# Optimization experiments

Measured on AMD Instinct MI355X. Metric: run time of the kernel, lower is better.

## Reference

```python
import jax, jax.numpy as jnp
import numpy as np

NUM_CLUSTERS = 32


def setup_inputs() -> dict:
    key = jax.random.key(0)
    k1, k2 = jax.random.split(key)
    B, N, D = 16, 16384, 128
    x = jax.random.normal(k1, (B, N, D), dtype=jnp.float32)
    cluster_ids = jax.random.randint(k2, (B, N), 0, NUM_CLUSTERS, dtype=jnp.int32)
    return {"x": x, "cluster_ids": cluster_ids}


def reference(x, cluster_ids):
    # x: [B, N, D]; cluster_ids: [B, N] int labels in [0, C)
    C = NUM_CLUSTERS
    # One-hot cluster membership: [B, N, C]
    onehot = (cluster_ids[..., None] == jnp.arange(C, dtype=cluster_ids.dtype)).astype(x.dtype)
    counts = onehot.sum(axis=1)                       # [B, C]
    sums = jnp.einsum('bnc,bnd->bcd', onehot, x)      # segment sums [B, C, D]
    # Per-cluster mean; empty clusters -> zero rows (contribute 0 to off-diag Gram)
    means = sums / jnp.maximum(counts, 1.0)[..., None]
    # Pairwise |dot products| between cluster means: [B, C, C]
    gram = jnp.abs(jnp.einsum('bcd,bed->bce', means, means))
    # Strict upper-triangular sum (torch.triu(..., diagonal=1))
    triu_mask = jnp.triu(jnp.ones((C, C), dtype=x.dtype), k=1)
    triu_sum = jnp.sum(gram * triu_mask, axis=(1, 2))  # [B]
    # Number of valid (non-empty) clusters per batch
    valid = jnp.sum(counts > 0, axis=1).astype(x.dtype)
    denom = jnp.where(valid > 1, valid * (valid - 1.0) * 0.5, 1.0)
    return jnp.mean(triu_sum / denom)
```

## Files before the change

### kernel.cpp

```cpp
#include <hip/hip_runtime.h>
#include <hip/hip_bf16.h>

#define BB 16
#define NN 16384
#define DD 128
#define CC 32
#define CHUNKS 32
#define NBLK (BB * CHUNKS)
#define ROWS_PER_BLOCK (NN / CHUNKS)
#define ROWS_PER_WAVE  (ROWS_PER_BLOCK / 4)

#define P_SUMS 0
#define P_CNTS ((size_t)NBLK * CC * DD)
#define R_SUMS (P_CNTS + (size_t)NBLK * CC)
#define R_CNTS (R_SUMS + (size_t)BB * CC * DD)
#define LOSSP  (R_CNTS + (size_t)BB * CC)
#define WS_A_FLOATS (LOSSP + BB)

__global__ __launch_bounds__(256) void seg_sum_kernel(
    const float* __restrict__ x, const int* __restrict__ ids,
    float* __restrict__ outsums, float* __restrict__ outcnts, int mode) {
  __shared__ float lsum[4][CC * DD];
  __shared__ float lcnt[CC];
  __shared__ int   lcid[ROWS_PER_BLOCK];

  const int tid  = threadIdx.x;
  const int b    = blockIdx.y;
  const int row0 = blockIdx.x * ROWS_PER_BLOCK;
  const int lane = tid & 63;
  const int w    = tid >> 6;
  const int slot = b * CHUNKS + blockIdx.x;
  const int* __restrict__ idrow = ids + (size_t)b * NN;

  if (tid < CC) lcnt[tid] = 0.f;
  lcid[tid]       = idrow[row0 + tid];
  lcid[tid + 256] = idrow[row0 + tid + 256];
  {
    const float4 z4 = make_float4(0.f, 0.f, 0.f, 0.f);
#pragma unroll
    for (int i = 0; i < 16; ++i)
      *reinterpret_cast<float4*>(&lsum[w][(i * 64 + lane) * 4]) = z4;
  }
  __syncthreads();
  atomicAdd(&lcnt[lcid[tid]], 1.f);
  atomicAdd(&lcnt[lcid[tid + 256]], 1.f);

  const float2* __restrict__ x2 =
      reinterpret_cast<const float2*>(x + (size_t)b * NN * DD);
  const int wbase = w * ROWS_PER_WAVE;
  float* const slab = &lsum[w][0];

  float2 vA[16], vB[16];
  int cA[16], cB[16];

#define LOADG(V, C, g)                                                     \
  {                                                                        \
    _Pragma("unroll") for (int k = 0; k < 16; ++k) {                       \
      const int rl = wbase + (g) * 16 + k;                                 \
      V[k] = x2[(size_t)(row0 + rl) * 64 + lane];                          \
      C[k] = lcid[rl];                                                     \
    }                                                                      \
  }
#define RMWG(V, C)                                                         \
  {                                                                        \
    _Pragma("unroll") for (int k = 0; k < 16; ++k) {                       \
      float2* p = reinterpret_cast<float2*>(&slab[C[k] * DD + 2 * lane]);  \
      float2 old = *p;                                                     \
      *p = make_float2(old.x + V[k].x, old.y + V[k].y);                    \
    }                                                                      \
  }

  LOADG(vA, cA, 0)
#pragma unroll
  for (int i = 0; i < 3; ++i) {
    LOADG(vB, cB, 2 * i + 1)
    RMWG(vA, cA)
    LOADG(vA, cA, 2 * i + 2)
    RMWG(vB, cB)
  }
  LOADG(vB, cB, 7)
  RMWG(vA, cA)
  RMWG(vB, cB)
#undef LOADG
#undef RMWG
  __syncthreads();

  if (mode) {
    float* __restrict__ ps = outsums + (size_t)slot * CC * DD;
#pragma unroll
    for (int it = 0; it < 4; ++it) {
      const int i = (it * 256 + tid) * 4;
      float4 s0 = *reinterpret_cast<const float4*>(&lsum[0][i]);
      float4 s1 = *reinterpret_cast<const float4*>(&lsum[1][i]);
      float4 s2 = *reinterpret_cast<const float4*>(&lsum[2][i]);
      float4 s3 = *reinterpret_cast<const float4*>(&lsum[3][i]);
      float4 r = make_float4(s0.x + s1.x + s2.x + s3.x, s0.y + s1.y + s2.y + s3.y,
                             s0.z + s1.z + s2.z + s3.z, s0.w + s1.w + s2.w + s3.w);
      *reinterpret_cast<float4*>(&ps[i]) = r;
    }
    if (tid < CC) outcnts[slot * CC + tid] = lcnt[tid];
  } else {
    float* __restrict__ gs = outsums + (size_t)b * CC * DD;
    for (int i = tid; i < CC * DD; i += 256) {
      float s = lsum[0][i] + lsum[1][i] + lsum[2][i] + lsum[3][i];
      atomicAdd(&gs[i], s);
    }
    if (tid < CC) atomicAdd(&outcnts[b * CC + tid], lcnt[tid]);
  }
}

__global__ __launch_bounds__(256) void reduce_partials_kernel(
    const float* __restrict__ psums, const float* __restrict__ pcnts,
    float* __restrict__ rsums, float* __restrict__ rcnts) {
  const int j = blockIdx.x;
  const int b = j >> 4;
  const int e0 = (j & 15) * 256;
  const int tid = threadIdx.x;
  float s = 0.f;
#pragma unroll 8
  for (int c = 0; c < CHUNKS; ++c)
    s += psums[((size_t)(b * CHUNKS + c)) * CC * DD + e0 + tid];
  rsums[(size_t)b * CC * DD + e0 + tid] = s;
  if ((j & 15) == 0 && tid < CC) {
    float cs = 0.f;
#pragma unroll 8
    for (int c = 0; c < CHUNKS; ++c) cs += pcnts[(b * CHUNKS + c) * CC + tid];
    rcnts[b * CC + tid] = cs;
  }
}

#define MSTR 132
__global__ __launch_bounds__(512) void finish_kernel(
    const float* __restrict__ gsums, const float* __restrict__ gcounts,
    float* __restrict__ lossp, float* __restrict__ out, int mode) {
  __shared__ float mean[CC * MSTR];
  __shared__ float cnt[CC];
  __shared__ float red[512];

  const int b = blockIdx.x;
  const int tid = threadIdx.x;

  if (tid < CC) cnt[tid] = gcounts[b * CC + tid];
  __syncthreads();

  for (int i = tid; i < CC * DD; i += 512) {
    int c = i >> 7;
    int d = i & 127;
    mean[c * MSTR + d] = gsums[(size_t)b * CC * DD + i] / fmaxf(cnt[c], 1.f);
  }
  __syncthreads();

  float acc = 0.f;
  if (tid < (CC * (CC - 1)) / 2) {
    int c = 0, rem = tid;
    while (rem >= (CC - 1 - c)) { rem -= (CC - 1 - c); ++c; }
    int e = c + 1 + rem;
    const float4* mc = reinterpret_cast<const float4*>(&mean[c * MSTR]);
    const float4* me = reinterpret_cast<const float4*>(&mean[e * MSTR]);
    float dot = 0.f;
#pragma unroll 8
    for (int j = 0; j < DD / 4; ++j) {
      float4 a = mc[j], bb = me[j];
      dot += a.x * bb.x + a.y * bb.y + a.z * bb.z + a.w * bb.w;
    }
    acc = fabsf(dot);
  }

  red[tid] = acc;
  __syncthreads();
  for (int s = 256; s > 0; s >>= 1) {
    if (tid < s) red[tid] += red[tid + s];
    __syncthreads();
  }

  if (tid == 0) {
    float valid = 0.f;
    for (int c = 0; c < CC; ++c) valid += (cnt[c] > 0.f) ? 1.f : 0.f;
    float denom = (valid > 1.f) ? valid * (valid - 1.f) * 0.5f : 1.f;
    float v = red[0] / denom * (1.0f / BB);
    if (mode) lossp[b] = v;
    else atomicAdd(out, v);
  }
}

__global__ __launch_bounds__(64) void final_kernel(
    const float* __restrict__ lossp, float* __restrict__ out) {
  float v = (threadIdx.x < BB) ? lossp[threadIdx.x] : 0.f;
#pragma unroll
  for (int o = 8; o > 0; o >>= 1) v += __shfl_down(v, o, 16);
  if (threadIdx.x == 0) out[0] = v;
}

extern "C" void kernel_launch(void* const* d_in, const int* in_sizes, int n_in,
                              void* d_out, int out_size, void* d_ws, size_t ws_size,
                              hipStream_t stream) {
  const float* x   = (const float*)d_in[0];
  const int*   ids = (const int*)d_in[1];
  float* out = (float*)d_out;
  float* ws  = (float*)d_ws;

  dim3 grid1(CHUNKS, BB);
  if (ws_size >= WS_A_FLOATS * sizeof(float)) {
    float* psums = ws + P_SUMS;
    float* pcnts = ws + P_CNTS;
    float* rsums = ws + R_SUMS;
    float* rcnts = ws + R_CNTS;
    float* lossp = ws + LOSSP;
    seg_sum_kernel<<<grid1, 256, 0, stream>>>(x, ids, psums, pcnts, 1);
    reduce_partials_kernel<<<256, 256, 0, stream>>>(psums, pcnts, rsums, rcnts);
    finish_kernel<<<BB, 512, 0, stream>>>(rsums, rcnts, lossp, out, 1);
    final_kernel<<<1, 64, 0, stream>>>(lossp, out);
  } else {
    float* gsums   = ws;
    float* gcounts = gsums + (size_t)BB * CC * DD;
    const size_t wsb = ((size_t)BB * CC * DD + (size_t)BB * CC) * sizeof(float);
    hipMemsetAsync(d_ws, 0, wsb, stream);
    hipMemsetAsync(d_out, 0, sizeof(float), stream);
    seg_sum_kernel<<<grid1, 256, 0, stream>>>(x, ids, gsums, gcounts, 0);
    finish_kernel<<<BB, 512, 0, stream>>>(gsums, gcounts, nullptr, out, 0);
  }
}
```

Baseline: 40.90 us.

## Fuse partial reduction and final loss into one finish kernel with atomic counter

Removes the separate reduce_partials and final kernels. The finish kernel now sums the 32 chunk partials itself, with 16 blocks each reading 512 KB. The last block to finish, detected through an atomic counter that seg_sum resets, writes the output. This cuts two launches and an intermediate global round trip, but the partial reduction now runs on only 16 blocks instead of 256, so it has less memory parallelism.

```diff
diff --git a/kernel.cpp b/kernel.cpp
--- a/kernel.cpp
+++ b/kernel.cpp
@@ -12,14 +12,14 @@
 
 #define P_SUMS 0
 #define P_CNTS ((size_t)NBLK * CC * DD)
-#define R_SUMS (P_CNTS + (size_t)NBLK * CC)
-#define R_CNTS (R_SUMS + (size_t)BB * CC * DD)
-#define LOSSP  (R_CNTS + (size_t)BB * CC)
-#define WS_A_FLOATS (LOSSP + BB)
+#define LOSSP  (P_CNTS + (size_t)NBLK * CC)
+#define CTR    (LOSSP + BB)
+#define WS_A_FLOATS (CTR + 1)
 
 __global__ __launch_bounds__(256) void seg_sum_kernel(
     const float* __restrict__ x, const int* __restrict__ ids,
-    float* __restrict__ outsums, float* __restrict__ outcnts, int mode) {
+    float* __restrict__ outsums, float* __restrict__ outcnts,
+    int* __restrict__ counter, int mode) {
   __shared__ float lsum[4][CC * DD];
   __shared__ float lcnt[CC];
   __shared__ int   lcid[ROWS_PER_BLOCK];
@@ -99,6 +99,8 @@
       *reinterpret_cast<float4*>(&ps[i]) = r;
     }
     if (tid < CC) outcnts[slot * CC + tid] = lcnt[tid];
+    if (slot == 0 && tid == 0)
+      __hip_atomic_store(counter, 0, __ATOMIC_RELAXED, __HIP_MEMORY_SCOPE_AGENT);
   } else {
     float* __restrict__ gs = outsums + (size_t)b * CC * DD;
     for (int i = tid; i < CC * DD; i += 256) {
@@ -109,44 +111,43 @@
   }
 }
 
-__global__ __launch_bounds__(256) void reduce_partials_kernel(
+#define MSTR 132
+__global__ __launch_bounds__(512) void finish_fused_kernel(
     const float* __restrict__ psums, const float* __restrict__ pcnts,
-    float* __restrict__ rsums, float* __restrict__ rcnts) {
-  const int j = blockIdx.x;
-  const int b = j >> 4;
-  const int e0 = (j & 15) * 256;
+    float* __restrict__ lossp, int* __restrict__ counter,
+    float* __restrict__ out) {
+  __shared__ float mean[CC * MSTR];
+  __shared__ float cnt[CC];
+  __shared__ float red[512];
+
+  const int b = blockIdx.x;
   const int tid = threadIdx.x;
-  float s = 0.f;
-#pragma unroll 8
-  for (int c = 0; c < CHUNKS; ++c)
-    s += psums[((size_t)(b * CHUNKS + c)) * CC * DD + e0 + tid];
-  rsums[(size_t)b * CC * DD + e0 + tid] = s;
-  if ((j & 15) == 0 && tid < CC) {
+
+  if (tid < CC) {
     float cs = 0.f;
 #pragma unroll 8
     for (int c = 0; c < CHUNKS; ++c) cs += pcnts[(b * CHUNKS + c) * CC + tid];
-    rcnts[b * CC + tid] = cs;
-  }
-}
-
-#define MSTR 132
-__global__ __launch_bounds__(512) void finish_kernel(
-    const float* __restrict__ gsums, const float* __restrict__ gcounts,
-    float* __restrict__ lossp, float* __restrict__ out, int mode) {
-  __shared__ float mean[CC * MSTR];
-  __shared__ float cnt[CC];
-  __shared__ float red[512];
-
-  const int b = blockIdx.x;
-  const int tid = threadIdx.x;
-
-  if (tid < CC) cnt[tid] = gcounts[b * CC + tid];
-  __syncthreads();
-
-  for (int i = tid; i < CC * DD; i += 512) {
-    int c = i >> 7;
-    int d = i & 127;
-    mean[c * MSTR + d] = gsums[(size_t)b * CC * DD + i] / fmaxf(cnt[c], 1.f);
+    cnt[tid] = cs;
+  }
+
+  float4 a0 = make_float4(0.f, 0.f, 0.f, 0.f), a1 = a0;
+  const size_t base = (size_t)b * CHUNKS * CC * DD + (size_t)tid * 8;
+#pragma unroll 4
+  for (int c = 0; c < CHUNKS; ++c) {
+    const float4* p = reinterpret_cast<const float4*>(&psums[base + (size_t)c * CC * DD]);
+    float4 q0 = p[0], q1 = p[1];
+    a0.x += q0.x; a0.y += q0.y; a0.z += q0.z; a0.w += q0.w;
+    a1.x += q1.x; a1.y += q1.y; a1.z += q1.z; a1.w += q1.w;
+  }
+  __syncthreads();
+
+  {
+    const int c = tid >> 4;
+    const int d0 = (tid & 15) * 8;
+    const float inv = 1.f / fmaxf(cnt[c], 1.f);
+    float* mrow = &mean[c * MSTR + d0];
+    mrow[0] = a0.x * inv; mrow[1] = a0.y * inv; mrow[2] = a0.z * inv; mrow[3] = a0.w * inv;
+    mrow[4] = a1.x * inv; mrow[5] = a1.y * inv; mrow[6] = a1.z * inv; mrow[7] = a1.w * inv;
   }
   __syncthreads();
 
@@ -160,8 +161,8 @@
     float dot = 0.f;
 #pragma unroll 8
     for (int j = 0; j < DD / 4; ++j) {
-      float4 a = mc[j], bb = me[j];
-      dot += a.x * bb.x + a.y * bb.y + a.z * bb.z + a.w * bb.w;
+      float4 u = mc[j], v = me[j];
+      dot += u.x * v.x + u.y * v.y + u.z * v.z + u.w * v.w;
     }
     acc = fabsf(dot);
   }
@@ -178,17 +179,70 @@
     for (int c = 0; c < CC; ++c) valid += (cnt[c] > 0.f) ? 1.f : 0.f;
     float denom = (valid > 1.f) ? valid * (valid - 1.f) * 0.5f : 1.f;
     float v = red[0] / denom * (1.0f / BB);
-    if (mode) lossp[b] = v;
-    else atomicAdd(out, v);
-  }
-}
-
-__global__ __launch_bounds__(64) void final_kernel(
-    const float* __restrict__ lossp, float* __restrict__ out) {
-  float v = (threadIdx.x < BB) ? lossp[threadIdx.x] : 0.f;
-#pragma unroll
-  for (int o = 8; o > 0; o >>= 1) v += __shfl_down(v, o, 16);
-  if (threadIdx.x == 0) out[0] = v;
+    __hip_atomic_store(&lossp[b], v, __ATOMIC_RELAXED, __HIP_MEMORY_SCOPE_AGENT);
+    __threadfence();
+    int old = __hip_atomic_fetch_add(counter, 1, __ATOMIC_ACQ_REL,
+                                     __HIP_MEMORY_SCOPE_AGENT);
+    if (old == BB - 1) {
+      float s = 0.f;
+#pragma unroll
+      for (int i = 0; i < BB; ++i)
+        s += __hip_atomic_load(&lossp[i], __ATOMIC_RELAXED,
+                               __HIP_MEMORY_SCOPE_AGENT);
+      out[0] = s;
+    }
+  }
+}
+
+__global__ __launch_bounds__(512) void finish_kernel_b(
+    const float* __restrict__ gsums, const float* __restrict__ gcounts,
+    float* __restrict__ out) {
+  __shared__ float mean[CC * MSTR];
+  __shared__ float cnt[CC];
+  __shared__ float red[512];
+
+  const int b = blockIdx.x;
+  const int tid = threadIdx.x;
+
+  if (tid < CC) cnt[tid] = gcounts[b * CC + tid];
+  __syncthreads();
+
+  for (int i = tid; i < CC * DD; i += 512) {
+    int c = i >> 7;
+    int d = i & 127;
+    mean[c * MSTR + d] = gsums[(size_t)b * CC * DD + i] / fmaxf(cnt[c], 1.f);
+  }
+  __syncthreads();
+
+  float acc = 0.f;
+  if (tid < (CC * (CC - 1)) / 2) {
+    int c = 0, rem = tid;
+    while (rem >= (CC - 1 - c)) { rem -= (CC - 1 - c); ++c; }
+    int e = c + 1 + rem;
+    const float4* mc = reinterpret_cast<const float4*>(&mean[c * MSTR]);
+    const float4* me = reinterpret_cast<const float4*>(&mean[e * MSTR]);
+    float dot = 0.f;
+#pragma unroll 8
+    for (int j = 0; j < DD / 4; ++j) {
+      float4 u = mc[j], v = me[j];
+      dot += u.x * v.x + u.y * v.y + u.z * v.z + u.w * v.w;
+    }
+    acc = fabsf(dot);
+  }
+
+  red[tid] = acc;
+  __syncthreads();
+  for (int s = 256; s > 0; s >>= 1) {
+    if (tid < s) red[tid] += red[tid + s];
+    __syncthreads();
+  }
+
+  if (tid == 0) {
+    float valid = 0.f;
+    for (int c = 0; c < CC; ++c) valid += (cnt[c] > 0.f) ? 1.f : 0.f;
+    float denom = (valid > 1.f) ? valid * (valid - 1.f) * 0.5f : 1.f;
+    atomicAdd(out, red[0] / denom * (1.0f / BB));
+  }
 }
 
 extern "C" void kernel_launch(void* const* d_in, const int* in_sizes, int n_in,
@@ -203,20 +257,17 @@
   if (ws_size >= WS_A_FLOATS * sizeof(float)) {
     float* psums = ws + P_SUMS;
     float* pcnts = ws + P_CNTS;
-    float* rsums = ws + R_SUMS;
-    float* rcnts = ws + R_CNTS;
     float* lossp = ws + LOSSP;
-    seg_sum_kernel<<<grid1, 256, 0, stream>>>(x, ids, psums, pcnts, 1);
-    reduce_partials_kernel<<<256, 256, 0, stream>>>(psums, pcnts, rsums, rcnts);
-    finish_kernel<<<BB, 512, 0, stream>>>(rsums, rcnts, lossp, out, 1);
-    final_kernel<<<1, 64, 0, stream>>>(lossp, out);
+    int*   ctr   = (int*)(ws + CTR);
+    seg_sum_kernel<<<grid1, 256, 0, stream>>>(x, ids, psums, pcnts, ctr, 1);
+    finish_fused_kernel<<<BB, 512, 0, stream>>>(psums, pcnts, lossp, ctr, out);
   } else {
     float* gsums   = ws;
     float* gcounts = gsums + (size_t)BB * CC * DD;
     const size_t wsb = ((size_t)BB * CC * DD + (size_t)BB * CC) * sizeof(float);
     hipMemsetAsync(d_ws, 0, wsb, stream);
     hipMemsetAsync(d_out, 0, sizeof(float), stream);
-    seg_sum_kernel<<<grid1, 256, 0, stream>>>(x, ids, gsums, gcounts, 0);
-    finish_kernel<<<BB, 512, 0, stream>>>(gsums, gcounts, nullptr, out, 0);
-  }
-}
+    seg_sum_kernel<<<grid1, 256, 0, stream>>>(x, ids, gsums, gcounts, nullptr, 0);
+    finish_kernel_b<<<BB, 512, 0, stream>>>(gsums, gcounts, out);
+  }
+}
```

Result: faster. 39.16 us (-4.2%).
